# Performance work log

Measured on AMD Instinct MI355X. Metric: run time of the kernel, lower is better.

The kernel has to match this reference:

```python
import jax, jax.numpy as jnp
import numpy as np

H, HD = 4, 32      # num_heads, head_dim
EPS = 1e-6         # flax LayerNorm default epsilon


def _ln(x, s, b):
    mu = jnp.mean(x, -1, keepdims=True)
    var = jnp.var(x, -1, keepdims=True)
    return (x - mu) * jax.lax.rsqrt(var + EPS) * s + b


def _pos_enc(T, D, dtype):
    # standard sinusoidal time-series positional encoding
    pos = jnp.arange(T, dtype=jnp.float32)[:, None]
    div = jnp.exp(-jnp.log(10000.0) * jnp.arange(0, D, 2, dtype=jnp.float32) / D)
    ang = pos * div
    pe = jnp.zeros((T, D), jnp.float32).at[:, 0::2].set(jnp.sin(ang)).at[:, 1::2].set(jnp.cos(ang))
    return pe.astype(dtype)


def _transformer(x, Wi, bi, Wqkv, bqkv, Wo, bo, l1s, l1b, l2s, l2b, W1, b1, W2, b2):
    # x: [B, T, in_dim] -> [B, T, D]; pre-LN transformer block with pos-enc
    B, T, _ = x.shape
    x = x @ Wi + bi
    D = x.shape[-1]
    x = x + _pos_enc(T, D, x.dtype)
    h = _ln(x, l1s, l1b)
    qkv = (h @ Wqkv + bqkv).reshape(B, T, 3, H, HD)
    q, k, v = qkv[:, :, 0], qkv[:, :, 1], qkv[:, :, 2]
    s = jnp.einsum('bthd,bshd->bhts', q, k) * (1.0 / np.sqrt(HD))
    o = jnp.einsum('bhts,bshd->bthd', jax.nn.softmax(s, -1), v).reshape(B, T, H * HD)
    x = x + (o @ Wo + bo)
    h = _ln(x, l2s, l2b)
    return x + jax.nn.gelu(h @ W1 + b1) @ W2 + b2


def _grand(h, Win, bin_, Wqk, bqk, Wout, bout, t_grid):
    # GRAND-style attention diffusion across node axis: dz/dt = (A(z) - I) z,
    # explicit Euler on the given time grid. h: [B, T, N, D]
    B, T, N, D = h.shape
    z = h @ Win + bin_
    dts = t_grid[1:] - t_grid[:-1]
    scale = 1.0 / np.sqrt(HD)
    for i in range(int(dts.shape[0])):
        qk = (z @ Wqk + bqk).reshape(B, T, N, 2, H, HD)
        q, k = qk[:, :, :, 0], qk[:, :, :, 1]
        s = jnp.einsum('btnhd,btmhd->bthnm', q, k) * scale
        A = jax.nn.softmax(s, -1).mean(axis=2)  # head-averaged [B, T, N, N]
        z = z + dts[i] * (jnp.einsum('btnm,btmd->btnd', A, z) - z)
    return z @ Wout + bout


def _forward(x, tt_Wi, tt_bi, tt_Wqkv, tt_bqkv, tt_Wo, tt_bo, tt_ln1s, tt_ln1b,
             tt_ln2s, tt_ln2b, tt_W1, tt_b1, tt_W2, tt_b2,
             g_Win, g_bin, g_Wqk, g_bqk, g_Wout, g_bout,
             ln_s, ln_b, mW1, mb1, mW2, mb2):
    # per-channel temporal transformer: vmap over node axis 2, params axis 0
    tmodel = jax.vmap(_transformer, in_axes=(2,) + (0,) * 14, out_axes=2)
    h = tmodel(x, tt_Wi, tt_bi, tt_Wqkv, tt_bqkv, tt_Wo, tt_bo,
               tt_ln1s, tt_ln1b, tt_ln2s, tt_ln2b, tt_W1, tt_b1, tt_W2, tt_b2)
    t_grid = jnp.linspace(0.0, 0.5, 4)
    h = _grand(h, g_Win, g_bin, g_Wqk, g_bqk, g_Wout, g_bout, t_grid)
    h2 = _ln(h, ln_s, ln_b)
    return jax.nn.gelu(h2 @ mW1 + mb1) @ mW2 + mb2


def setup_inputs() -> dict:
    key = jax.random.key(0)
    ks = iter(jax.random.split(key, 32))
    B, T, N, IN, D = 8, 128, 64, 32, 128
    w = lambda shape: jax.random.normal(next(ks), shape, jnp.float32) * 0.02
    z = lambda shape: jnp.zeros(shape, jnp.float32)
    o = lambda shape: jnp.ones(shape, jnp.float32)
    return dict(
        x=jax.random.normal(next(ks), (B, T, N, IN), jnp.float32),
        tt_Wi=w((N, IN, D)), tt_bi=z((N, D)),
        tt_Wqkv=w((N, D, 3 * H * HD)), tt_bqkv=z((N, 3 * H * HD)),
        tt_Wo=w((N, H * HD, D)), tt_bo=z((N, D)),
        tt_ln1s=o((N, D)), tt_ln1b=z((N, D)),
        tt_ln2s=o((N, D)), tt_ln2b=z((N, D)),
        tt_W1=w((N, D, D)), tt_b1=z((N, D)),
        tt_W2=w((N, D, D)), tt_b2=z((N, D)),
        g_Win=w((D, D)), g_bin=z((D,)),
        g_Wqk=w((D, 2 * H * HD)), g_bqk=z((2 * H * HD,)),
        g_Wout=w((D, D)), g_bout=z((D,)),
        ln_s=o((D,)), ln_b=z((D,)),
        mW1=w((D, D)), mb1=z((D,)),
        mW2=w((D, D)), mb2=z((D,)),
    )


def reference(x, tt_Wi, tt_bi, tt_Wqkv, tt_bqkv, tt_Wo, tt_bo, tt_ln1s, tt_ln1b,
              tt_ln2s, tt_ln2b, tt_W1, tt_b1, tt_W2, tt_b2,
              g_Win, g_bin, g_Wqk, g_bqk, g_Wout, g_bout,
              ln_s, ln_b, mW1, mb1, mW2, mb2):
    return _forward(x, tt_Wi, tt_bi, tt_Wqkv, tt_bqkv, tt_Wo, tt_bo, tt_ln1s, tt_ln1b,
                    tt_ln2s, tt_ln2b, tt_W1, tt_b1, tt_W2, tt_b2,
                    g_Win, g_bin, g_Wqk, g_bqk, g_Wout, g_bout,
                    ln_s, ln_b, mW1, mb1, mW2, mb2)
```

## Files before the change

### kernel.cpp

```cpp
#include <hip/hip_runtime.h>
#include <hip/hip_bf16.h>

using bf16 = __hip_bfloat16;
typedef __attribute__((ext_vector_type(8))) short short8;
typedef __attribute__((ext_vector_type(4))) float f32x4;


__device__ __forceinline__ bool isbf(const void* p) {
    return *(const unsigned*)p == 0x3F803F80u;
}
template <bool BF>
__device__ __forceinline__ float ldT(const void* p, size_t i) {
    if constexpr (BF) return __bfloat162float(((const bf16*)p)[i]);
    else              return ((const float*)p)[i];
}
template <bool BF>
__device__ __forceinline__ void stT(void* p, size_t i, float v) {
    if constexpr (BF) ((bf16*)p)[i] = __float2bfloat16(v);
    else              ((float*)p)[i] = v;
}
template <bool BF>
__device__ __forceinline__ unsigned ldbits(const void* p, size_t i) {
    if constexpr (BF) return ((const unsigned short*)p)[i];
    else {
        union { bf16 h; unsigned short u; } c;
        c.h = __float2bfloat16(((const float*)p)[i]);
        return c.u;
    }
}
__device__ __forceinline__ float b2f(bf16 x) { return __bfloat162float(x); }
__device__ __forceinline__ bf16  f2b(float x) { return __float2bfloat16(x); }
__device__ __forceinline__ unsigned short f2bu(float x) {
    union { bf16 h; unsigned short u; } c; c.h = f2b(x); return c.u;
}
__device__ __forceinline__ float bu2f(unsigned short u) {
    union { bf16 h; unsigned short u; } c; c.u = u; return b2f(c.h);
}
template <bool BF>
__device__ __forceinline__ float2 ld2T(const void* p, size_t i) {
    if constexpr (BF) {
        unsigned u = *(const unsigned*)((const unsigned short*)p + i);
        return make_float2(bu2f((unsigned short)(u & 0xffff)),
                           bu2f((unsigned short)(u >> 16)));
    } else {
        return *(const float2*)((const float*)p + i);
    }
}
__device__ __forceinline__ short8 u4_to_s8(uint4 u) {
    union { uint4 u; short8 s; } c; c.u = u; return c.s;
}
__device__ __forceinline__ unsigned pack2(float a, float b) {
    return (unsigned)f2bu(a) | ((unsigned)f2bu(b) << 16);
}
__device__ __forceinline__ float gelu_f(float x) {
    float t = fmaf(x * x * x, 0.0713548162f, 1.5957691216f * x);
    return x / (1.0f + __expf(-t));
}

template <bool BF>
__device__ __forceinline__ void ln_afrags(
    const float* __restrict__ rp, const void* __restrict__ lnsP,
    const void* __restrict__ lnbP, size_t pb, int lg, short8 af[4])
{
    float e[4][8];
    float sum = 0.f, sq = 0.f;
#pragma unroll
    for (int kk = 0; kk < 4; ++kk) {
        float4 fa = *(const float4*)(rp + 32 * kk + 8 * lg);
        float4 fb = *(const float4*)(rp + 32 * kk + 8 * lg + 4);
        e[kk][0] = fa.x; e[kk][1] = fa.y; e[kk][2] = fa.z; e[kk][3] = fa.w;
        e[kk][4] = fb.x; e[kk][5] = fb.y; e[kk][6] = fb.z; e[kk][7] = fb.w;
#pragma unroll
        for (int j = 0; j < 8; ++j) {
            sum += e[kk][j];
            sq  += e[kk][j] * e[kk][j];
        }
    }
    sum += __shfl_xor(sum, 16); sum += __shfl_xor(sum, 32);
    sq  += __shfl_xor(sq, 16);  sq  += __shfl_xor(sq, 32);
    float mu = sum * (1.0f / 128.0f);
    float var = sq * (1.0f / 128.0f) - mu * mu;
    float rs = rsqrtf(var + 1e-6f);
#pragma unroll
    for (int kk = 0; kk < 4; ++kk) {
        unsigned dw[4];
#pragma unroll
        for (int p = 0; p < 4; ++p) {
            int col = 32 * kk + 8 * lg + 2 * p;
            float2 sv = ld2T<BF>(lnsP, pb + col);
            float2 bv = ld2T<BF>(lnbP, pb + col);
            dw[p] = pack2((e[kk][2 * p]     - mu) * rs * sv.x + bv.x,
                          (e[kk][2 * p + 1] - mu) * rs * sv.y + bv.y);
        }
        af[kk] = u4_to_s8(make_uint4(dw[0], dw[1], dw[2], dw[3]));
    }
}

struct PrepArgs {
    const void* W[10];
    uint4* Wf[10];
    float* pe;
};
__device__ __constant__ const int prep_KK[10]    = {4,4,4,4,4,4,4,4,4,1};
__device__ __constant__ const int prep_NT[10]    = {24,8,8,8,8,16,8,8,8,8};
__device__ __constant__ const int prep_start[11] =
    {0,6144,8192,10240,12288,12320,12384,12416,12448,12480,12992};

template <bool BF>
__device__ __forceinline__ void prep_body(PrepArgs a) {
    int bid = blockIdx.x;
    int l = threadIdx.x;
    if (bid >= 12992) {
        int t = bid - 12992;
        int d = l * 2;
        float div0 = expf(-9.210340371976184f * (float)(d & ~1) * (1.0f / 128.0f));
        float ang = (float)t * div0;
        *(float2*)(a.pe + t * 128 + d) = make_float2(sinf(ang), cosf(ang));
        return;
    }
    int seg = 0;
#pragma unroll
    for (int s = 1; s < 10; ++s) seg += (bid >= prep_start[s]);
    int local = bid - prep_start[seg];
    int KK = prep_KK[seg], NT = prep_NT[seg];
    int kk = local % KK;
    int nt = (local / KK) % NT;
    int node = local / (KK * NT);
    int Nout = NT * 16;
    int lg = l >> 4, li = l & 15;
    int col = nt * 16 + li;
    int k0 = kk * 32 + lg * 8;
    size_t base = (size_t)node * (KK * 32) * Nout;
    const void* W = a.W[seg];
    unsigned w[4];
#pragma unroll
    for (int p = 0; p < 4; ++p) {
        unsigned lo = ldbits<BF>(W, base + (size_t)(k0 + 2 * p) * Nout + col);
        unsigned hi = ldbits<BF>(W, base + (size_t)(k0 + 2 * p + 1) * Nout + col);
        w[p] = lo | (hi << 16);
    }
    a.Wf[seg][(((size_t)node * NT + nt) * KK + kk) * 64 + l] =
        make_uint4(w[0], w[1], w[2], w[3]);
}
__global__ __launch_bounds__(64) void k_prep(PrepArgs a, const void* probe) {
    if (isbf(probe)) prep_body<true>(a);
    else             prep_body<false>(a);
}

template <bool ADD, bool PERM, bool BF>
__device__ __forceinline__ void mgemm_body(
    const uint4* __restrict__ A, const uint4* __restrict__ Wf,
    const void* __restrict__ Bias, const float* __restrict__ AddF,
    float* __restrict__ OutF, int Nout, int NT, int nodeW, int nodeB)
{
    int n64 = blockIdx.y, node = blockIdx.z;
    int row_base = blockIdx.z * 1024 + blockIdx.x * 64;
    int l = threadIdx.x, lg = l >> 4, li = l & 15;
    int wnode = nodeW ? node : 0;

    short8 bfrag[4][4];
    const uint4* wp = Wf + (((size_t)wnode * NT + n64 * 4) * 4) * 64 + l;
#pragma unroll
    for (int nt = 0; nt < 4; ++nt)
#pragma unroll
        for (int kk = 0; kk < 4; ++kk)
            bfrag[nt][kk] = u4_to_s8(wp[(nt * 4 + kk) * 64]);

    float bias[4];
#pragma unroll
    for (int nt = 0; nt < 4; ++nt)
        bias[nt] = ldT<BF>(Bias, (size_t)(nodeB ? node : 0) * Nout +
                                     n64 * 64 + nt * 16 + li);

#pragma unroll
    for (int m4 = 0; m4 < 4; ++m4) {
        int arow = row_base + m4 * 16 + li;
        short8 af[4];
        const uint4* ap = A + (size_t)arow * 16;
#pragma unroll
        for (int kk = 0; kk < 4; ++kk) af[kk] = u4_to_s8(ap[kk * 4 + lg]);
        f32x4 acc[4];
#pragma unroll
        for (int nt = 0; nt < 4; ++nt) {
            acc[nt] = (f32x4){0.f, 0.f, 0.f, 0.f};
#pragma unroll
            for (int kk = 0; kk < 4; ++kk)
                acc[nt] = __builtin_amdgcn_mfma_f32_16x16x32_bf16(
                    af[kk], bfrag[nt][kk], acc[nt], 0, 0, 0);
        }
#pragma unroll
        for (int nt = 0; nt < 4; ++nt) {
            int j = n64 * 64 + nt * 16 + li;
#pragma unroll
            for (int s = 0; s < 4; ++s) {
                int orow = row_base + m4 * 16 + (lg << 2) + s;
                int r_out = PERM ? ((orow & 1023) * 64 + (orow >> 10)) : orow;
                size_t oi = (size_t)r_out * Nout + j;
                float v = acc[nt][s] + bias[nt];
                if constexpr (ADD) v += AddF[oi];
                OutF[oi] = v;
            }
        }
    }
}
template <bool ADD, bool PERM>
__global__ __launch_bounds__(64) void k_mgemm(
    const uint4* A, const uint4* Wf, const void* Bias, const float* AddF,
    float* OutF, int Nout, int NT, int nodeW, int nodeB, const void* probe)
{
    if (isbf(probe))
        mgemm_body<ADD, PERM, true>(A, Wf, Bias, AddF, OutF, Nout, NT, nodeW, nodeB);
    else
        mgemm_body<ADD, PERM, false>(A, Wf, Bias, AddF, OutF, Nout, NT, nodeW, nodeB);
}

template <bool BF>
__device__ __forceinline__ void qkv_body(
    const float* __restrict__ X, const void* __restrict__ l1s,
    const void* __restrict__ l1b, const uint4* __restrict__ Wf,
    const void* __restrict__ Bias, unsigned short* __restrict__ Out)
{
    int tile = blockIdx.x, node = blockIdx.z;
    int l = threadIdx.x, lg = l >> 4, li = l & 15;

    short8 af[4][4];
#pragma unroll
    for (int m4 = 0; m4 < 4; ++m4) {
        int q = tile * 64 + m4 * 16 + li;
        ln_afrags<BF>(X + ((size_t)q * 64 + node) * 128, l1s, l1b,
                      (size_t)node * 128, lg, af[m4]);
    }
#pragma unroll
    for (int ct = 0; ct < 6; ++ct) {
        short8 bfr[4][4];
        float bias[4];
#pragma unroll
        for (int nt = 0; nt < 4; ++nt) {
#pragma unroll
            for (int kk = 0; kk < 4; ++kk)
                bfr[nt][kk] = u4_to_s8(Wf[(((size_t)node * 24 + ct * 4 + nt) * 4 + kk) * 64 + l]);
            bias[nt] = ldT<BF>(Bias, (size_t)node * 384 + ct * 64 + nt * 16 + li);
        }
#pragma unroll
        for (int m4 = 0; m4 < 4; ++m4) {
            f32x4 acc[4];
#pragma unroll
            for (int nt = 0; nt < 4; ++nt) {
                acc[nt] = (f32x4){0.f, 0.f, 0.f, 0.f};
#pragma unroll
                for (int kk = 0; kk < 4; ++kk)
                    acc[nt] = __builtin_amdgcn_mfma_f32_16x16x32_bf16(
                        af[m4][kk], bfr[nt][kk], acc[nt], 0, 0, 0);
            }
#pragma unroll
            for (int nt = 0; nt < 4; ++nt) {
                int j = ct * 64 + nt * 16 + li;
#pragma unroll
                for (int s = 0; s < 4; ++s) {
                    int orow = node * 1024 + tile * 64 + m4 * 16 + (lg << 2) + s;
                    Out[(size_t)orow * 384 + j] = f2bu(acc[nt][s] + bias[nt]);
                }
            }
        }
    }
}
__global__ __launch_bounds__(64) void k_qkv(
    const float* X, const void* l1s, const void* l1b, const uint4* Wf,
    const void* Bias, unsigned short* Out, const void* probe)
{
    if (isbf(probe)) qkv_body<true>(X, l1s, l1b, Wf, Bias, Out);
    else             qkv_body<false>(X, l1s, l1b, Wf, Bias, Out);
}

template <bool BF>
__device__ __forceinline__ void ffn_body(
    float* __restrict__ X, const void* __restrict__ l2s,
    const void* __restrict__ l2b, const uint4* __restrict__ W1f,
    const void* __restrict__ b1, const uint4* __restrict__ W2f,
    const void* __restrict__ b2, const uint4* __restrict__ Ginf,
    const void* __restrict__ gbin, unsigned short* __restrict__ Hs,
    unsigned short* __restrict__ Rs)
{
    int tile = blockIdx.x, node = blockIdx.z;
    int tid = threadIdx.x;
    int w = tid >> 6;
    int l = tid & 63, lg = l >> 4, li = l & 15;

    {
        short8 bfr[2][4];
        float biasv[2];
#pragma unroll
        for (int t2 = 0; t2 < 2; ++t2) {
            int nt = 2 * w + t2;
#pragma unroll
            for (int kk = 0; kk < 4; ++kk)
                bfr[t2][kk] = u4_to_s8(W1f[(((size_t)node * 8 + nt) * 4 + kk) * 64 + l]);
            biasv[t2] = ldT<BF>(b1, (size_t)node * 128 + nt * 16 + li);
        }
#pragma unroll
        for (int m4 = 0; m4 < 4; ++m4) {
            int q = tile * 64 + m4 * 16 + li;
            short8 af[4];
            ln_afrags<BF>(X + ((size_t)q * 64 + node) * 128, l2s, l2b,
                          (size_t)node * 128, lg, af);
#pragma unroll
            for (int t2 = 0; t2 < 2; ++t2) {
                int nt = 2 * w + t2;
                f32x4 acc = (f32x4){0.f, 0.f, 0.f, 0.f};
#pragma unroll
                for (int kk = 0; kk < 4; ++kk)
                    acc = __builtin_amdgcn_mfma_f32_16x16x32_bf16(
                        af[kk], bfr[t2][kk], acc, 0, 0, 0);
                int j = nt * 16 + li;
#pragma unroll
                for (int s = 0; s < 4; ++s) {
                    int row = m4 * 16 + (lg << 2) + s;
                    Hs[row * 128 + (j ^ ((row & 7) << 3))] =
                        f2bu(gelu_f(acc[s] + biasv[t2]));
                }
            }
        }
    }
    __syncthreads();
    {
        short8 bfr[2][4];
        float biasv[2];
#pragma unroll
        for (int t2 = 0; t2 < 2; ++t2) {
            int nt = 2 * w + t2;
#pragma unroll
            for (int kk = 0; kk < 4; ++kk)
                bfr[t2][kk] = u4_to_s8(W2f[(((size_t)node * 8 + nt) * 4 + kk) * 64 + l]);
            biasv[t2] = ldT<BF>(b2, (size_t)node * 128 + nt * 16 + li);
        }
#pragma unroll
        for (int m4 = 0; m4 < 4; ++m4) {
            short8 af[4];
#pragma unroll
            for (int kk = 0; kk < 4; ++kk)
                af[kk] = u4_to_s8(*(const uint4*)&Hs[(16 * m4 + li) * 128 +
                                 ((32 * kk + 8 * lg) ^ ((li & 7) << 3))]);
#pragma unroll
            for (int t2 = 0; t2 < 2; ++t2) {
                int nt = 2 * w + t2;
                f32x4 acc = (f32x4){0.f, 0.f, 0.f, 0.f};
#pragma unroll
                for (int kk = 0; kk < 4; ++kk)
                    acc = __builtin_amdgcn_mfma_f32_16x16x32_bf16(
                        af[kk], bfr[t2][kk], acc, 0, 0, 0);
                int j = nt * 16 + li;
#pragma unroll
                for (int s = 0; s < 4; ++s) {
                    int row = m4 * 16 + (lg << 2) + s;
                    int q = tile * 64 + row;
                    float v = acc[s] + biasv[t2] +
                              X[((size_t)q * 64 + node) * 128 + j];
                    Rs[row * 128 + (j ^ ((row & 7) << 3))] = f2bu(v);
                }
            }
        }
    }
    __syncthreads();
    {
        short8 bfr[2][4];
        float biasv[2];
#pragma unroll
        for (int t2 = 0; t2 < 2; ++t2) {
            int nt = 2 * w + t2;
#pragma unroll
            for (int kk = 0; kk < 4; ++kk)
                bfr[t2][kk] = u4_to_s8(Ginf[((size_t)nt * 4 + kk) * 64 + l]);
            biasv[t2] = ldT<BF>(gbin, nt * 16 + li);
        }
#pragma unroll
        for (int m4 = 0; m4 < 4; ++m4) {
            short8 af[4];
#pragma unroll
            for (int kk = 0; kk < 4; ++kk)
                af[kk] = u4_to_s8(*(const uint4*)&Rs[(16 * m4 + li) * 128 +
                                 ((32 * kk + 8 * lg) ^ ((li & 7) << 3))]);
#pragma unroll
            for (int t2 = 0; t2 < 2; ++t2) {
                int nt = 2 * w + t2;
                f32x4 acc = (f32x4){0.f, 0.f, 0.f, 0.f};
#pragma unroll
                for (int kk = 0; kk < 4; ++kk)
                    acc = __builtin_amdgcn_mfma_f32_16x16x32_bf16(
                        af[kk], bfr[t2][kk], acc, 0, 0, 0);
                int j = nt * 16 + li;
#pragma unroll
                for (int s = 0; s < 4; ++s) {
                    int row = m4 * 16 + (lg << 2) + s;
                    int q = tile * 64 + row;
                    X[((size_t)q * 64 + node) * 128 + j] = acc[s] + biasv[t2];
                }
            }
        }
    }
}
__global__ __launch_bounds__(256) void k_ffn(
    float* X, const void* l2s, const void* l2b, const uint4* W1f,
    const void* b1, const uint4* W2f, const void* b2, const uint4* Ginf,
    const void* gbin, const void* probe)
{
    __shared__ unsigned short Hs[64 * 128];
    __shared__ unsigned short Rs[64 * 128];
    if (isbf(probe)) ffn_body<true>(X, l2s, l2b, W1f, b1, W2f, b2, Ginf, gbin, Hs, Rs);
    else             ffn_body<false>(X, l2s, l2b, W1f, b1, W2f, b2, Ginf, gbin, Hs, Rs);
}

template <bool BF>
__device__ __forceinline__ void head_body(
    const float* __restrict__ X, const void* __restrict__ lns,
    const void* __restrict__ lnb, const uint4* __restrict__ M1f,
    const void* __restrict__ mb1, const uint4* __restrict__ M2f,
    const void* __restrict__ mb2, void* __restrict__ Out,
    unsigned short* __restrict__ Hs)
{
    int row_base = blockIdx.x * 64;
    int tid = threadIdx.x;
    int w = tid >> 6;
    int l = tid & 63, lg = l >> 4, li = l & 15;

    {
        short8 bfr[2][4];
        float biasv[2];
#pragma unroll
        for (int t2 = 0; t2 < 2; ++t2) {
            int nt = 2 * w + t2;
#pragma unroll
            for (int kk = 0; kk < 4; ++kk)
                bfr[t2][kk] = u4_to_s8(M1f[((size_t)nt * 4 + kk) * 64 + l]);
            biasv[t2] = ldT<BF>(mb1, nt * 16 + li);
        }
#pragma unroll
        for (int m4 = 0; m4 < 4; ++m4) {
            int arow = row_base + m4 * 16 + li;
            short8 af[4];
            ln_afrags<BF>(X + (size_t)arow * 128, lns, lnb, 0, lg, af);
#pragma unroll
            for (int t2 = 0; t2 < 2; ++t2) {
                int nt = 2 * w + t2;
                f32x4 acc = (f32x4){0.f, 0.f, 0.f, 0.f};
#pragma unroll
                for (int kk = 0; kk < 4; ++kk)
                    acc = __builtin_amdgcn_mfma_f32_16x16x32_bf16(
                        af[kk], bfr[t2][kk], acc, 0, 0, 0);
                int j = nt * 16 + li;
#pragma unroll
                for (int s = 0; s < 4; ++s) {
                    int row = m4 * 16 + (lg << 2) + s;
                    Hs[row * 128 + (j ^ ((row & 7) << 3))] =
                        f2bu(gelu_f(acc[s] + biasv[t2]));
                }
            }
        }
    }
    __syncthreads();
    {
        short8 bfr[2][4];
        float biasv[2];
#pragma unroll
        for (int t2 = 0; t2 < 2; ++t2) {
            int nt = 2 * w + t2;
#pragma unroll
            for (int kk = 0; kk < 4; ++kk)
                bfr[t2][kk] = u4_to_s8(M2f[((size_t)nt * 4 + kk) * 64 + l]);
            biasv[t2] = ldT<BF>(mb2, nt * 16 + li);
        }
#pragma unroll
        for (int m4 = 0; m4 < 4; ++m4) {
            short8 af[4];
#pragma unroll
            for (int kk = 0; kk < 4; ++kk)
                af[kk] = u4_to_s8(*(const uint4*)&Hs[(16 * m4 + li) * 128 +
                                 ((32 * kk + 8 * lg) ^ ((li & 7) << 3))]);
#pragma unroll
            for (int t2 = 0; t2 < 2; ++t2) {
                int nt = 2 * w + t2;
                f32x4 acc = (f32x4){0.f, 0.f, 0.f, 0.f};
#pragma unroll
                for (int kk = 0; kk < 4; ++kk)
                    acc = __builtin_amdgcn_mfma_f32_16x16x32_bf16(
                        af[kk], bfr[t2][kk], acc, 0, 0, 0);
                int j = nt * 16 + li;
#pragma unroll
                for (int s = 0; s < 4; ++s) {
                    int orow = row_base + m4 * 16 + (lg << 2) + s;
                    stT<BF>(Out, (size_t)orow * 128 + j, acc[s] + biasv[t2]);
                }
            }
        }
    }
}
__global__ __launch_bounds__(256) void k_head(
    const float* X, const void* lns, const void* lnb, const uint4* M1f,
    const void* mb1, const uint4* M2f, const void* mb2, void* Out,
    const void* probe)
{
    __shared__ unsigned short Hs[64 * 128];
    if (isbf(probe)) head_body<true>(X, lns, lnb, M1f, mb1, M2f, mb2, Out, Hs);
    else             head_body<false>(X, lns, lnb, M1f, mb1, M2f, mb2, Out, Hs);
}

template <bool BF>
__device__ __forceinline__ void inproj_mfma_body(
    const void* __restrict__ x, const uint4* __restrict__ WfWi,
    const void* __restrict__ bi, const float* __restrict__ pe,
    float* __restrict__ X)
{
    int tile = blockIdx.x, n64 = blockIdx.y, node = blockIdx.z;
    int l = threadIdx.x, lg = l >> 4, li = l & 15;

    short8 bfrag[4];
    float bias[4];
#pragma unroll
    for (int nt = 0; nt < 4; ++nt) {
        bfrag[nt] = u4_to_s8(WfWi[((size_t)node * 8 + n64 * 4 + nt) * 64 + l]);
        bias[nt] = ldT<BF>(bi, (size_t)node * 128 + n64 * 64 + nt * 16 + li);
    }

#pragma unroll
    for (int mt = 0; mt < 4; ++mt) {
        int q = tile * 64 + mt * 16 + li;
        size_t xoff = ((size_t)q * 64 + node) * 32 + 8 * lg;
        short8 af;
        if constexpr (BF) {
            af = u4_to_s8(*(const uint4*)((const unsigned short*)x + xoff));
        } else {
            float4 fa = *(const float4*)((const float*)x + xoff);
            float4 fb = *(const float4*)((const float*)x + xoff + 4);
            af = u4_to_s8(make_uint4(pack2(fa.x, fa.y), pack2(fa.z, fa.w),
                                     pack2(fb.x, fb.y), pack2(fb.z, fb.w)));
        }
        f32x4 acc[4];
#pragma unroll
        for (int nt = 0; nt < 4; ++nt)
            acc[nt] = __builtin_amdgcn_mfma_f32_16x16x32_bf16(
                af, bfrag[nt], (f32x4){0.f, 0.f, 0.f, 0.f}, 0, 0, 0);
#pragma unroll
        for (int nt = 0; nt < 4; ++nt) {
            int j = n64 * 64 + nt * 16 + li;
#pragma unroll
            for (int s = 0; s < 4; ++s) {
                int qo = tile * 64 + mt * 16 + (lg << 2) + s;
                size_t oi = ((size_t)qo * 64 + node) * 128 + j;
                X[oi] = acc[nt][s] + bias[nt] + pe[(qo & 127) * 128 + j];
            }
        }
    }
}
__global__ __launch_bounds__(64) void k_inproj_mfma(
    const void* x, const uint4* WfWi, const void* bi, const float* pe,
    float* X, const void* probe)
{
    if (isbf(probe)) inproj_mfma_body<true>(x, WfWi, bi, pe, X);
    else             inproj_mfma_body<false>(x, WfWi, bi, pe, X);
}

__global__ __launch_bounds__(128, 2) void k_attn(
    const unsigned short* __restrict__ QKV, bf16* __restrict__ O)
{
    int bid = blockIdx.x;
    int h = bid & 3;
    int b = (bid >> 2) & 7;
    int n = bid >> 5;
    int l = threadIdx.x & 63;
    int wv = threadIdx.x >> 6;
    int lg = l >> 4, li = l & 15;
    const float scale = 0.17677669529663687f;

    size_t panel = ((size_t)n * 1024 + b * 128) * 384;

    short8 kf[8];
#pragma unroll
    for (int kt = 0; kt < 8; ++kt) {
        const uint4* p = (const uint4*)(QKV + panel + (size_t)(kt * 16 + li) * 384
                                        + 128 + h * 32 + 8 * lg);
        kf[kt] = u4_to_s8(*p);
    }
    short8 vf[2][4];
#pragma unroll
    for (int dt = 0; dt < 2; ++dt)
#pragma unroll
        for (int kc = 0; kc < 4; ++kc) {
            unsigned dw[4];
#pragma unroll
            for (int p = 0; p < 4; ++p) {
                int t0 = kc * 32 + 8 * lg + 2 * p;
                unsigned u0 = QKV[panel + (size_t)t0 * 384 + 256 + h * 32 + dt * 16 + li];
                unsigned u1 = QKV[panel + (size_t)(t0 + 1) * 384 + 256 + h * 32 + dt * 16 + li];
                dw[p] = u0 | (u1 << 16);
            }
            vf[dt][kc] = u4_to_s8(make_uint4(dw[0], dw[1], dw[2], dw[3]));
        }

#pragma unroll
    for (int ss = 0; ss < 4; ++ss) {
        int st = wv * 4 + ss;
        const uint4* qp = (const uint4*)(QKV + panel + (size_t)(st * 16 + li) * 384
                                         + h * 32 + 8 * lg);
        short8 qf = u4_to_s8(*qp);

        f32x4 sa[8];
#pragma unroll
        for (int kt = 0; kt < 8; ++kt)
            sa[kt] = __builtin_amdgcn_mfma_f32_16x16x32_bf16(
                kf[kt], qf, (f32x4){0.f, 0.f, 0.f, 0.f}, 0, 0, 0);

        float m = -1e30f;
#pragma unroll
        for (int kt = 0; kt < 8; ++kt)
#pragma unroll
            for (int s = 0; s < 4; ++s) {
                sa[kt][s] *= scale;
                m = fmaxf(m, sa[kt][s]);
            }
        m = fmaxf(m, __shfl_xor(m, 16));
        m = fmaxf(m, __shfl_xor(m, 32));
        float lsum = 0.f;
#pragma unroll
        for (int kt = 0; kt < 8; ++kt)
#pragma unroll
            for (int s = 0; s < 4; ++s) {
                float e = __expf(sa[kt][s] - m);
                sa[kt][s] = e;
                lsum += e;
            }
        lsum += __shfl_xor(lsum, 16);
        lsum += __shfl_xor(lsum, 32);

        unsigned pdw[8][2];
#pragma unroll
        for (int kt = 0; kt < 8; ++kt) {
            pdw[kt][0] = pack2(sa[kt][0], sa[kt][1]);
            pdw[kt][1] = pack2(sa[kt][2], sa[kt][3]);
        }

        f32x4 o0 = (f32x4){0.f, 0.f, 0.f, 0.f};
        f32x4 o1 = (f32x4){0.f, 0.f, 0.f, 0.f};
#pragma unroll
        for (int kc = 0; kc < 4; ++kc) {
            unsigned bd[4];
#pragma unroll
            for (int j = 0; j < 4; ++j) {
                int src = (2 * (lg & 1) + (j >> 1)) * 16 + li;
                unsigned v0 = (unsigned)__shfl((int)pdw[2 * kc][j & 1], src);
                unsigned v1 = (unsigned)__shfl((int)pdw[2 * kc + 1][j & 1], src);
                bd[j] = (lg & 2) ? v1 : v0;
            }
            short8 pf = u4_to_s8(make_uint4(bd[0], bd[1], bd[2], bd[3]));
            o0 = __builtin_amdgcn_mfma_f32_16x16x32_bf16(vf[0][kc], pf, o0, 0, 0, 0);
            o1 = __builtin_amdgcn_mfma_f32_16x16x32_bf16(vf[1][kc], pf, o1, 0, 0, 0);
        }
        float linv = 1.0f / lsum;
        size_t obase = ((size_t)n * 1024 + b * 128 + st * 16 + li) * 128 + h * 32;
        uint2 w0, w1;
        w0.x = pack2(o0[0] * linv, o0[1] * linv);
        w0.y = pack2(o0[2] * linv, o0[3] * linv);
        w1.x = pack2(o1[0] * linv, o1[1] * linv);
        w1.y = pack2(o1[2] * linv, o1[3] * linv);
        *(uint2*)((unsigned short*)O + obase + 4 * lg)      = w0;
        *(uint2*)((unsigned short*)O + obase + 16 + 4 * lg) = w1;
    }
}

template <bool BF>
__device__ __forceinline__ void grand_fused_body(
    float* __restrict__ Xf, const uint4* __restrict__ Wqk,
    const void* __restrict__ bqk, const uint4* __restrict__ Goutf,
    const void* __restrict__ gbout,
    unsigned short* __restrict__ Zb, unsigned short* __restrict__ QKs)
{
    int bt = blockIdx.x;
    int tid = threadIdx.x;
    int w = tid >> 6;
    int h = w >> 1, wh = w & 1;
    int l = tid & 63, lg = l >> 4, li = l & 15;
    const float scale = 0.17677669529663687f;
    const float dtv = 0.16666667f;
    const int dcol = 16 * w + li;

    float zreg[4][4];
#pragma unroll
    for (int nt = 0; nt < 4; ++nt)
#pragma unroll
        for (int s = 0; s < 4; ++s) {
            int n = 16 * nt + 4 * lg + s;
            float z = Xf[((size_t)bt * 64 + n) * 128 + dcol];
            zreg[nt][s] = z;
            Zb[n * 128 + (dcol ^ ((n & 7) << 3))] = f2bu(z);
        }
    float bias[2];
#pragma unroll
    for (int jt = 0; jt < 2; ++jt)
        bias[jt] = ldT<BF>(bqk, 32 * w + 16 * jt + li);
    __syncthreads();

    for (int it = 0; it < 3; ++it) {
#pragma unroll
        for (int jt = 0; jt < 2; ++jt) {
            short8 bfr[4];
#pragma unroll
            for (int kk = 0; kk < 4; ++kk)
                bfr[kk] = u4_to_s8(Wqk[(((2 * w + jt) * 4) + kk) * 64 + l]);
#pragma unroll
            for (int mt = 0; mt < 4; ++mt) {
                short8 af[4];
#pragma unroll
                for (int kk = 0; kk < 4; ++kk)
                    af[kk] = u4_to_s8(*(const uint4*)&Zb[(16 * mt + li) * 128 +
                                     ((32 * kk + 8 * lg) ^ ((li & 7) << 3))]);
                f32x4 acc = (f32x4){0.f, 0.f, 0.f, 0.f};
#pragma unroll
                for (int kk = 0; kk < 4; ++kk)
                    acc = __builtin_amdgcn_mfma_f32_16x16x32_bf16(
                        af[kk], bfr[kk], acc, 0, 0, 0);
#pragma unroll
                for (int s = 0; s < 4; ++s) {
                    int row = 16 * mt + 4 * lg + s;
                    QKs[row * 256 + ((32 * w + 16 * jt + li) ^ ((row & 7) << 3))] =
                        f2bu(acc[s] + bias[jt]);
                }
            }
        }
        __syncthreads();
        short8 kf[4], qf[2];
#pragma unroll
        for (int kt = 0; kt < 4; ++kt)
            kf[kt] = u4_to_s8(*(const uint4*)&QKs[(16 * kt + li) * 256 +
                              ((128 + 32 * h + 8 * lg) ^ ((li & 7) << 3))]);
#pragma unroll
        for (int j = 0; j < 2; ++j)
            qf[j] = u4_to_s8(*(const uint4*)&QKs[(16 * (2 * wh + j) + li) * 256 +
                             ((32 * h + 8 * lg) ^ ((li & 7) << 3))]);
        __syncthreads();

        f32x4 sa[4][2];
#pragma unroll
        for (int kt = 0; kt < 4; ++kt)
#pragma unroll
            for (int j = 0; j < 2; ++j)
                sa[kt][j] = __builtin_amdgcn_mfma_f32_16x16x32_bf16(
                    kf[kt], qf[j], (f32x4){0.f, 0.f, 0.f, 0.f}, 0, 0, 0);
        float mx[2], sm[2];
#pragma unroll
        for (int j = 0; j < 2; ++j) mx[j] = -1e30f;
#pragma unroll
        for (int kt = 0; kt < 4; ++kt)
#pragma unroll
            for (int j = 0; j < 2; ++j)
#pragma unroll
                for (int s = 0; s < 4; ++s) {
                    sa[kt][j][s] *= scale;
                    mx[j] = fmaxf(mx[j], sa[kt][j][s]);
                }
#pragma unroll
        for (int j = 0; j < 2; ++j) {
            mx[j] = fmaxf(mx[j], __shfl_xor(mx[j], 16));
            mx[j] = fmaxf(mx[j], __shfl_xor(mx[j], 32));
            sm[j] = 0.f;
        }
#pragma unroll
        for (int kt = 0; kt < 4; ++kt)
#pragma unroll
            for (int j = 0; j < 2; ++j)
#pragma unroll
                for (int s = 0; s < 4; ++s) {
                    float e = __expf(sa[kt][j][s] - mx[j]);
                    sa[kt][j][s] = e;
                    sm[j] += e;
                }
#pragma unroll
        for (int j = 0; j < 2; ++j) {
            sm[j] += __shfl_xor(sm[j], 16);
            sm[j] += __shfl_xor(sm[j], 32);
            sm[j] = 0.25f / sm[j];
        }
#pragma unroll
        for (int kt = 0; kt < 4; ++kt)
#pragma unroll
            for (int j = 0; j < 2; ++j) {
                int q = 16 * (2 * wh + j) + li;
                int col0 = 64 * h + 16 * kt + 4 * lg;
                int ix = q * 256 + (col0 ^ ((q & 7) << 3));
                *(unsigned*)&QKs[ix]     = pack2(sa[kt][j][0] * sm[j],
                                                 sa[kt][j][1] * sm[j]);
                *(unsigned*)&QKs[ix + 2] = pack2(sa[kt][j][2] * sm[j],
                                                 sa[kt][j][3] * sm[j]);
            }
        __syncthreads();
        unsigned pz[4][2];
#pragma unroll
        for (int nt = 0; nt < 4; ++nt) {
            pz[nt][0] = pack2(zreg[nt][0], zreg[nt][1]);
            pz[nt][1] = pack2(zreg[nt][2], zreg[nt][3]);
        }
        short8 bz[2];
#pragma unroll
        for (int kk = 0; kk < 2; ++kk) {
            unsigned dw[4];
#pragma unroll
            for (int p = 0; p < 4; ++p) {
                int src = ((2 * lg + (p >> 1)) & 3) * 16 + li;
                unsigned v0 = (unsigned)__shfl((int)pz[2 * kk][p & 1], src);
                unsigned v1 = (unsigned)__shfl((int)pz[2 * kk + 1][p & 1], src);
                dw[p] = (lg & 2) ? v1 : v0;
            }
            bz[kk] = u4_to_s8(make_uint4(dw[0], dw[1], dw[2], dw[3]));
        }
        f32x4 oz[4];
#pragma unroll
        for (int nt = 0; nt < 4; ++nt) oz[nt] = (f32x4){0.f, 0.f, 0.f, 0.f};
#pragma unroll
        for (int hh = 0; hh < 4; ++hh)
#pragma unroll
            for (int kk = 0; kk < 2; ++kk)
#pragma unroll
                for (int nt = 0; nt < 4; ++nt) {
                    short8 af = u4_to_s8(*(const uint4*)&QKs[(16 * nt + li) * 256 +
                                 ((64 * hh + 32 * kk + 8 * lg) ^ ((li & 7) << 3))]);
                    oz[nt] = __builtin_amdgcn_mfma_f32_16x16x32_bf16(
                        af, bz[kk], oz[nt], 0, 0, 0);
                }
#pragma unroll
        for (int nt = 0; nt < 4; ++nt)
#pragma unroll
            for (int s = 0; s < 4; ++s) {
                int n = 16 * nt + 4 * lg + s;
                float z = zreg[nt][s];
                float zn = z + dtv * (oz[nt][s] - z);
                zreg[nt][s] = zn;
                Zb[n * 128 + (dcol ^ ((n & 7) << 3))] = f2bu(zn);
            }
        __syncthreads();
    }
    {
        float* QKf = (float*)QKs;
        short8 gb[4];
#pragma unroll
        for (int kk = 0; kk < 4; ++kk)
            gb[kk] = u4_to_s8(Goutf[((size_t)w * 4 + kk) * 64 + l]);
        float gbias = ldT<BF>(gbout, 16 * w + li);
#pragma unroll
        for (int mt = 0; mt < 4; ++mt) {
            short8 af[4];
#pragma unroll
            for (int kk = 0; kk < 4; ++kk)
                af[kk] = u4_to_s8(*(const uint4*)&Zb[(16 * mt + li) * 128 +
                                 ((32 * kk + 8 * lg) ^ ((li & 7) << 3))]);
            f32x4 acc = (f32x4){0.f, 0.f, 0.f, 0.f};
#pragma unroll
            for (int kk = 0; kk < 4; ++kk)
                acc = __builtin_amdgcn_mfma_f32_16x16x32_bf16(
                    af[kk], gb[kk], acc, 0, 0, 0);
#pragma unroll
            for (int s = 0; s < 4; ++s) {
                int n = 16 * mt + 4 * lg + s;
                QKf[n * 128 + 16 * w + li] = acc[s] + gbias;
            }
        }
        __syncthreads();
        for (int idx = tid; idx < 2048; idx += 512) {
            int row = idx >> 5, c = idx & 31;
            ((float4*)Xf)[((size_t)bt * 64 + row) * 32 + c] =
                ((const float4*)QKf)[row * 32 + c];
        }
    }
}
__global__ __launch_bounds__(512, 2) void k_grand_fused(
    float* Xf, const uint4* Wqk, const void* bqk, const uint4* Goutf,
    const void* gbout, const void* probe)
{
    __shared__ unsigned short Zb[64 * 128];
    __shared__ unsigned short QKs[64 * 256];
    if (isbf(probe)) grand_fused_body<true>(Xf, Wqk, bqk, Goutf, gbout, Zb, QKs);
    else             grand_fused_body<false>(Xf, Wqk, bqk, Goutf, gbout, Zb, QKs);
}

extern "C" void kernel_launch(void* const* d_in, const int* in_sizes, int n_in,
                              void* d_out, int out_size, void* d_ws, size_t ws_size,
                              hipStream_t stream)
{
    const void* x     = d_in[0];
    const void* tWi   = d_in[1];
    const void* tbi   = d_in[2];
    const void* tWqkv = d_in[3];
    const void* tbqkv = d_in[4];
    const void* tWo   = d_in[5];
    const void* tbo   = d_in[6];
    const void* l1s   = d_in[7];
    const void* l1b   = d_in[8];
    const void* l2s   = d_in[9];
    const void* l2b   = d_in[10];
    const void* tW1   = d_in[11];
    const void* tb1   = d_in[12];
    const void* tW2   = d_in[13];
    const void* tb2   = d_in[14];
    const void* gWin  = d_in[15];
    const void* gbin  = d_in[16];
    const void* gWqk  = d_in[17];
    const void* gbqk  = d_in[18];
    const void* gWout = d_in[19];
    const void* gbout = d_in[20];
    const void* lns   = d_in[21];
    const void* lnb   = d_in[22];
    const void* mW1   = d_in[23];
    const void* mb1   = d_in[24];
    const void* mW2   = d_in[25];
    const void* mb2   = d_in[26];
    const void* probe = lns;

    const size_t MiB = 1u << 20;
    char* ws = (char*)d_ws;

    float* X   = (float*)ws;
    float* pe  = (float*)(ws + 61 * MiB);
    bf16*  S16 = (bf16*)(ws + 64 * MiB);
    bf16*  bfA = (bf16*)(ws + 112 * MiB);

    char* wf = ws + 32 * MiB;
    uint4* WfQKV = (uint4*)(wf);
    uint4* WfWo  = (uint4*)(wf + 6291456);
    uint4* WfW1  = (uint4*)(wf + 8388608);
    uint4* WfW2  = (uint4*)(wf + 10485760);
    uint4* WfGin = (uint4*)(wf + 12582912);
    uint4* WfGqk = (uint4*)(wf + 12615680);
    uint4* WfGout= (uint4*)(wf + 12681216);
    uint4* WfM1  = (uint4*)(wf + 12713984);
    uint4* WfM2  = (uint4*)(wf + 12746752);
    uint4* WfWi  = (uint4*)(wf + 12779520);

    PrepArgs pa;
    pa.W[0] = tWqkv; pa.Wf[0] = WfQKV;
    pa.W[1] = tWo;   pa.Wf[1] = WfWo;
    pa.W[2] = tW1;   pa.Wf[2] = WfW1;
    pa.W[3] = tW2;   pa.Wf[3] = WfW2;
    pa.W[4] = gWin;  pa.Wf[4] = WfGin;
    pa.W[5] = gWqk;  pa.Wf[5] = WfGqk;
    pa.W[6] = gWout; pa.Wf[6] = WfGout;
    pa.W[7] = mW1;   pa.Wf[7] = WfM1;
    pa.W[8] = mW2;   pa.Wf[8] = WfM2;
    pa.W[9] = tWi;   pa.Wf[9] = WfWi;
    pa.pe = pe;
    k_prep<<<13120, 64, 0, stream>>>(pa, probe);

    k_inproj_mfma<<<dim3(16, 2, 64), 64, 0, stream>>>(x, WfWi, tbi, pe, X, probe);
    k_qkv<<<dim3(16, 1, 64), 64, 0, stream>>>(
        X, l1s, l1b, WfQKV, tbqkv, (unsigned short*)S16, probe);
    k_attn<<<2048, 128, 0, stream>>>((const unsigned short*)S16, bfA);
    k_mgemm<true, true><<<dim3(16, 2, 64), 64, 0, stream>>>(
        (const uint4*)bfA, WfWo, tbo, X, X, 128, 8, 1, 1, probe);
    k_ffn<<<dim3(16, 1, 64), 256, 0, stream>>>(
        X, l2s, l2b, WfW1, tb1, WfW2, tb2, WfGin, gbin, probe);

    k_grand_fused<<<1024, 512, 0, stream>>>(X, WfGqk, gbqk, WfGout, gbout, probe);

    k_head<<<1024, 256, 0, stream>>>(
        X, lns, lnb, WfM1, mb1, WfM2, mb2, d_out, probe);
}
```

Baseline: 238.4 us.

## Stage LayerNorm rows once in LDS and share across waves in qkv/ffn/head

The LayerNorm of each 64-row tile is now computed once, with each wave handling 16 rows, and written as bf16 A-fragments into swizzled shared memory. In the ffn and head kernels this removes the redundant LN recomputation that every wave did before. The qkv kernel grows from one wave per block to six, each producing one 64-column slice of the 384 outputs. This gives far more parallelism for that kernel but adds a block barrier and extra LDS use. In the ffn kernel the LN staging reuses the Rs buffer, which is only safe if Rs is not read again before this point.

Measured after the change: 213.8 us (median of 2 runs). -10.3%, faster.

```diff
diff --git a/kernel.cpp b/kernel.cpp
--- a/kernel.cpp
+++ b/kernel.cpp
@@ -49,6 +49,9 @@
 __device__ __forceinline__ short8 u4_to_s8(uint4 u) {
     union { uint4 u; short8 s; } c; c.u = u; return c.s;
 }
+__device__ __forceinline__ uint4 s8_to_u4(short8 s) {
+    union { uint4 u; short8 s; } c; c.s = s; return c.u;
+}
 __device__ __forceinline__ unsigned pack2(float a, float b) {
     return (unsigned)f2bu(a) | ((unsigned)f2bu(b) << 16);
 }
@@ -94,6 +97,20 @@
         }
         af[kk] = u4_to_s8(make_uint4(dw[0], dw[1], dw[2], dw[3]));
     }
+}
+
+template <bool BF>
+__device__ __forceinline__ void ln_stage16(
+    const float* __restrict__ Xbase, size_t rowStride, int row0,
+    const void* __restrict__ lnsP, const void* __restrict__ lnbP, size_t pb,
+    int lg, int li, unsigned short* __restrict__ As)
+{
+    short8 af[4];
+    ln_afrags<BF>(Xbase + (size_t)(row0 + li) * rowStride, lnsP, lnbP, pb, lg, af);
+#pragma unroll
+    for (int kk = 0; kk < 4; ++kk)
+        *(uint4*)&As[(row0 + li) % 64 * 128 +
+                     ((32 * kk + 8 * lg) ^ ((li & 7) << 3))] = s8_to_u4(af[kk]);
 }
 
 struct PrepArgs {
@@ -218,58 +235,64 @@
 __device__ __forceinline__ void qkv_body(
     const float* __restrict__ X, const void* __restrict__ l1s,
     const void* __restrict__ l1b, const uint4* __restrict__ Wf,
-    const void* __restrict__ Bias, unsigned short* __restrict__ Out)
+    const void* __restrict__ Bias, unsigned short* __restrict__ Out,
+    unsigned short* __restrict__ As)
 {
     int tile = blockIdx.x, node = blockIdx.z;
-    int l = threadIdx.x, lg = l >> 4, li = l & 15;
-
-    short8 af[4][4];
+    int tid = threadIdx.x;
+    int w = tid / 64;
+    int l = tid & 63, lg = l >> 4, li = l & 15;
+
+    if (w < 4)
+        ln_stage16<BF>(X + (size_t)node * 128, 64 * 128,
+                       tile * 64 + w * 16, l1s, l1b, (size_t)node * 128,
+                       lg, li, As);
+    __syncthreads();
+
+    int ct = w;
+    short8 bfr[4][4];
+    float bias[4];
+#pragma unroll
+    for (int nt = 0; nt < 4; ++nt) {
+#pragma unroll
+        for (int kk = 0; kk < 4; ++kk)
+            bfr[nt][kk] = u4_to_s8(Wf[(((size_t)node * 24 + ct * 4 + nt) * 4 + kk) * 64 + l]);
+        bias[nt] = ldT<BF>(Bias, (size_t)node * 384 + ct * 64 + nt * 16 + li);
+    }
 #pragma unroll
     for (int m4 = 0; m4 < 4; ++m4) {
-        int q = tile * 64 + m4 * 16 + li;
-        ln_afrags<BF>(X + ((size_t)q * 64 + node) * 128, l1s, l1b,
-                      (size_t)node * 128, lg, af[m4]);
-    }
-#pragma unroll
-    for (int ct = 0; ct < 6; ++ct) {
-        short8 bfr[4][4];
-        float bias[4];
+        short8 af[4];
+#pragma unroll
+        for (int kk = 0; kk < 4; ++kk)
+            af[kk] = u4_to_s8(*(const uint4*)&As[(16 * m4 + li) * 128 +
+                             ((32 * kk + 8 * lg) ^ ((li & 7) << 3))]);
+        f32x4 acc[4];
 #pragma unroll
         for (int nt = 0; nt < 4; ++nt) {
-#pragma unroll
-            for (int kk = 0; kk < 4; ++kk)
-                bfr[nt][kk] = u4_to_s8(Wf[(((size_t)node * 24 + ct * 4 + nt) * 4 + kk) * 64 + l]);
-            bias[nt] = ldT<BF>(Bias, (size_t)node * 384 + ct * 64 + nt * 16 + li);
-        }
-#pragma unroll
-        for (int m4 = 0; m4 < 4; ++m4) {
-            f32x4 acc[4];
-#pragma unroll
-            for (int nt = 0; nt < 4; ++nt) {
-                acc[nt] = (f32x4){0.f, 0.f, 0.f, 0.f};
-#pragma unroll
-                for (int kk = 0; kk < 4; ++kk)
-                    acc[nt] = __builtin_amdgcn_mfma_f32_16x16x32_bf16(
-                        af[m4][kk], bfr[nt][kk], acc[nt], 0, 0, 0);
-            }
-#pragma unroll
-            for (int nt = 0; nt < 4; ++nt) {
-                int j = ct * 64 + nt * 16 + li;
-#pragma unroll
-                for (int s = 0; s < 4; ++s) {
-                    int orow = node * 1024 + tile * 64 + m4 * 16 + (lg << 2) + s;
-                    Out[(size_t)orow * 384 + j] = f2bu(acc[nt][s] + bias[nt]);
-                }
-            }
-        }
-    }
-}
-__global__ __launch_bounds__(64) void k_qkv(
+            acc[nt] = (f32x4){0.f, 0.f, 0.f, 0.f};
+#pragma unroll
+            for (int kk = 0; kk < 4; ++kk)
+                acc[nt] = __builtin_amdgcn_mfma_f32_16x16x32_bf16(
+                    af[kk], bfr[nt][kk], acc[nt], 0, 0, 0);
+        }
+#pragma unroll
+        for (int nt = 0; nt < 4; ++nt) {
+            int j = ct * 64 + nt * 16 + li;
+#pragma unroll
+            for (int s = 0; s < 4; ++s) {
+                int orow = node * 1024 + tile * 64 + m4 * 16 + (lg << 2) + s;
+                Out[(size_t)orow * 384 + j] = f2bu(acc[nt][s] + bias[nt]);
+            }
+        }
+    }
+}
+__global__ __launch_bounds__(384) void k_qkv(
     const float* X, const void* l1s, const void* l1b, const uint4* Wf,
     const void* Bias, unsigned short* Out, const void* probe)
 {
-    if (isbf(probe)) qkv_body<true>(X, l1s, l1b, Wf, Bias, Out);
-    else             qkv_body<false>(X, l1s, l1b, Wf, Bias, Out);
+    __shared__ unsigned short As[64 * 128];
+    if (isbf(probe)) qkv_body<true>(X, l1s, l1b, Wf, Bias, Out, As);
+    else             qkv_body<false>(X, l1s, l1b, Wf, Bias, Out, As);
 }
 
 template <bool BF>
@@ -286,6 +309,9 @@
     int w = tid >> 6;
     int l = tid & 63, lg = l >> 4, li = l & 15;
 
+    ln_stage16<BF>(X + (size_t)node * 128, 64 * 128,
+                   tile * 64 + w * 16, l2s, l2b, (size_t)node * 128, lg, li, Rs);
+    __syncthreads();
     {
         short8 bfr[2][4];
         float biasv[2];
@@ -299,10 +325,11 @@
         }
 #pragma unroll
         for (int m4 = 0; m4 < 4; ++m4) {
-            int q = tile * 64 + m4 * 16 + li;
             short8 af[4];
-            ln_afrags<BF>(X + ((size_t)q * 64 + node) * 128, l2s, l2b,
-                          (size_t)node * 128, lg, af);
+#pragma unroll
+            for (int kk = 0; kk < 4; ++kk)
+                af[kk] = u4_to_s8(*(const uint4*)&Rs[(16 * m4 + li) * 128 +
+                                 ((32 * kk + 8 * lg) ^ ((li & 7) << 3))]);
 #pragma unroll
             for (int t2 = 0; t2 < 2; ++t2) {
                 int nt = 2 * w + t2;
@@ -415,13 +442,15 @@
     const void* __restrict__ lnb, const uint4* __restrict__ M1f,
     const void* __restrict__ mb1, const uint4* __restrict__ M2f,
     const void* __restrict__ mb2, void* __restrict__ Out,
-    unsigned short* __restrict__ Hs)
+    unsigned short* __restrict__ Hs, unsigned short* __restrict__ As)
 {
     int row_base = blockIdx.x * 64;
     int tid = threadIdx.x;
     int w = tid >> 6;
     int l = tid & 63, lg = l >> 4, li = l & 15;
 
+    ln_stage16<BF>(X, 128, row_base + w * 16, lns, lnb, 0, lg, li, As);
+    __syncthreads();
     {
         short8 bfr[2][4];
         float biasv[2];
@@ -435,9 +464,11 @@
         }
 #pragma unroll
         for (int m4 = 0; m4 < 4; ++m4) {
-            int arow = row_base + m4 * 16 + li;
             short8 af[4];
-            ln_afrags<BF>(X + (size_t)arow * 128, lns, lnb, 0, lg, af);
+#pragma unroll
+            for (int kk = 0; kk < 4; ++kk)
+                af[kk] = u4_to_s8(*(const uint4*)&As[(16 * m4 + li) * 128 +
+                                 ((32 * kk + 8 * lg) ^ ((li & 7) << 3))]);
 #pragma unroll
             for (int t2 = 0; t2 < 2; ++t2) {
                 int nt = 2 * w + t2;
@@ -499,8 +530,9 @@
     const void* probe)
 {
     __shared__ unsigned short Hs[64 * 128];
-    if (isbf(probe)) head_body<true>(X, lns, lnb, M1f, mb1, M2f, mb2, Out, Hs);
-    else             head_body<false>(X, lns, lnb, M1f, mb1, M2f, mb2, Out, Hs);
+    __shared__ unsigned short As[64 * 128];
+    if (isbf(probe)) head_body<true>(X, lns, lnb, M1f, mb1, M2f, mb2, Out, Hs, As);
+    else             head_body<false>(X, lns, lnb, M1f, mb1, M2f, mb2, Out, Hs, As);
 }
 
 template <bool BF>
@@ -946,7 +978,7 @@
     k_prep<<<13120, 64, 0, stream>>>(pa, probe);
 
     k_inproj_mfma<<<dim3(16, 2, 64), 64, 0, stream>>>(x, WfWi, tbi, pe, X, probe);
-    k_qkv<<<dim3(16, 1, 64), 64, 0, stream>>>(
+    k_qkv<<<dim3(16, 1, 64), 384, 0, stream>>>(
         X, l1s, l1b, WfQKV, tbqkv, (unsigned short*)S16, probe);
     k_attn<<<2048, 128, 0, stream>>>((const unsigned short*)S16, bfA);
     k_mgemm<true, true><<<dim3(16, 2, 64), 64, 0, stream>>>(
```
